# Kernel tuning notes

Measured on AMD Instinct MI355X. Metric: run time of the kernel, lower is better.

Reference implementation:

```python
import jax, jax.numpy as jnp
import numpy as np

N, L, H, E = 4, 4096, 8, 64
CHUNK = 128  # chunk size for the blocked causal scan
EPS = 1e-6


def elu_feature_map(x):
    # phi(x) = elu(x) + 1 (default feature map of fast-transformers)
    return jax.nn.elu(x) + 1.0


def causal_dot_product(Q, K, V, chunk=CHUNK):
    """out[n,l,h,:] = sum_{s<=l} (Q[n,l,h,:].K[n,s,h,:]) * V[n,s,h,:].
    Chunked scan over the [E,M] KV state: O(N L H E M) without an [L,L] matrix."""
    n, l, h, e = Q.shape
    m = V.shape[-1]
    nc = l // chunk

    def to_chunks(x):
        # [n, l, h, d] -> [nc, n, h, chunk, d]
        return x.reshape(n, nc, chunk, h, x.shape[-1]).transpose(1, 0, 3, 2, 4)

    q, k, v = to_chunks(Q), to_chunks(K), to_chunks(V)
    tril = jnp.tril(jnp.ones((chunk, chunk), dtype=Q.dtype))

    def step(S, xs):  # S: [n, h, e, m] running sum of k v^T
        qc, kc, vc = xs  # [n, h, chunk, e/m]
        inter = jnp.einsum('nhce,nhem->nhcm', qc, S)
        attn = jnp.einsum('nhce,nhde->nhcd', qc, kc) * tril  # intra-chunk causal
        intra = jnp.einsum('nhcd,nhdm->nhcm', attn, vc)
        S = S + jnp.einsum('nhce,nhcm->nhem', kc, vc)
        return S, inter + intra

    S0 = jnp.zeros((n, h, e, m), dtype=Q.dtype)
    _, out = jax.lax.scan(step, S0, (q, k, v))  # [nc, n, h, chunk, m]
    return out.transpose(1, 0, 3, 2, 4).reshape(n, l, h, m)


def setup_inputs() -> dict:
    key = jax.random.key(0)
    k1, k2, k3 = jax.random.split(key, 3)
    return {
        'queries': jax.random.normal(k1, (N, L, H, E), jnp.float32),
        'keys': jax.random.normal(k2, (N, L, H, E), jnp.float32),
        'values': jax.random.normal(k3, (N, L, H, E), jnp.float32),
        'key_lengths': jnp.ones((N, L), jnp.float32),  # float length mask
    }


def reference(queries, keys, values, key_lengths):
    Q = elu_feature_map(queries)
    K = elu_feature_map(keys) * key_lengths[:, :, None, None]
    # denominator: Z[n,l,h] = 1 / (Q[n,l,h] . cumsum_s<=l K[n,s,h] + eps)
    Z = 1.0 / (jnp.einsum('nlhe,nlhe->nlh', Q, jnp.cumsum(K, axis=1)) + EPS)
    V_new = causal_dot_product(Q, K, values)
    return V_new * Z[:, :, :, None]
```

## Files before the change

kernel.cpp:

```cpp
#include <hip/hip_runtime.h>
#include <math.h>

#define NN 4
#define LL 4096
#define HH 8
#define EE 64
#define CHK 128
#define SUB 64
#define NCH (LL/CHK)
#define NG (NN*HH*NCH)
#define EPSF 1e-6f

typedef float f32x4 __attribute__((ext_vector_type(4)));
typedef __bf16 bf16x8 __attribute__((ext_vector_type(8)));

__device__ __forceinline__ float phi_map(float x) {
  return x > 0.0f ? x + 1.0f : __expf(x);
}

#define MFMA(a, b, c) __builtin_amdgcn_mfma_f32_16x16x32_bf16((a), (b), (c), 0, 0, 0)

__device__ __forceinline__ int swz(int row, int d) {
  return row * 128 + (d & 7) + 8 * ((d >> 3) ^ ((row >> 2) & 7));
}
__device__ __forceinline__ int frag_off(int row, int ks, int lg) {
  return row * 128 + 8 * ((4 * ks + lg) ^ ((row >> 2) & 7));
}

__global__ __launch_bounds__(256) void k_chunksums(
    const float* __restrict__ Kg, const float* __restrict__ Vg,
    const float* __restrict__ KLg, __bf16* __restrict__ ScG, __bf16* __restrict__ KscG)
{
  __shared__ __bf16 sKt[64 * 128];
  __shared__ __bf16 sVt[64 * 128];
  const int g = blockIdx.x;
  const int c = g % NCH;
  const int nh = g / NCH;
  const int h = nh % HH;
  const int n = nh / HH;
  const int l0 = c * CHK;
  const int t = threadIdx.x;

  #pragma unroll
  for (int it = 0; it < 8; ++it) {
    int f = t + 256 * it;
    int d = f >> 4;
    int c4 = (f & 15) << 2;
    size_t gb = (((size_t)n * LL + (size_t)(l0 + d)) * HH + h) * EE + c4;
    float4 kk = *(const float4*)(Kg + gb);
    float4 vv = *(const float4*)(Vg + gb);
    float klr = KLg[n * LL + l0 + d];
    float ka[4] = {phi_map(kk.x) * klr, phi_map(kk.y) * klr,
                   phi_map(kk.z) * klr, phi_map(kk.w) * klr};
    float va[4] = {vv.x, vv.y, vv.z, vv.w};
    #pragma unroll
    for (int j = 0; j < 4; ++j) {
      sKt[swz(c4 + j, d)] = (__bf16)ka[j];
      sVt[swz(c4 + j, d)] = (__bf16)va[j];
    }
  }
  __syncthreads();

  const int w = t >> 6;
  const int lane = t & 63;
  const int lg = lane >> 4;
  const int li = lane & 15;

  bf16x8 aV[4];
  #pragma unroll
  for (int ks = 0; ks < 4; ++ks)
    aV[ks] = *(const bf16x8*)&sVt[frag_off(16 * w + li, ks, lg)];

  bf16x8 ones;
  #pragma unroll
  for (int i = 0; i < 8; ++i) ones[i] = (__bf16)1.0f;

  f32x4 acc[4], accK[4];
  #pragma unroll
  for (int nt = 0; nt < 4; ++nt) {
    acc[nt] = (f32x4){0.f, 0.f, 0.f, 0.f};
    accK[nt] = (f32x4){0.f, 0.f, 0.f, 0.f};
  }

  #pragma unroll
  for (int nt = 0; nt < 4; ++nt) {
    #pragma unroll
    for (int ks = 0; ks < 4; ++ks) {
      bf16x8 b = *(const bf16x8*)&sKt[frag_off(li + 16 * nt, ks, lg)];
      acc[nt] = MFMA(aV[ks], b, acc[nt]);
      if (w == 0) accK[nt] = MFMA(ones, b, accK[nt]);
    }
  }

  __bf16* sp = ScG + (size_t)g * 4096;
  #pragma unroll
  for (int nt = 0; nt < 4; ++nt)
    #pragma unroll
    for (int reg = 0; reg < 4; ++reg)
      sp[(16 * w + 4 * lg + reg) * 64 + li + 16 * nt] = (__bf16)acc[nt][reg];

  if (w == 0 && lg == 0) {
    #pragma unroll
    for (int nt = 0; nt < 4; ++nt)
      KscG[(size_t)g * 64 + li + 16 * nt] = (__bf16)accK[nt][0];
  }
}

__global__ __launch_bounds__(256) void k_prefix(
    const __bf16* __restrict__ Sc, __bf16* __restrict__ Sp,
    const __bf16* __restrict__ Ksc, __bf16* __restrict__ Ksp)
{
  const int bid = blockIdx.x;
  const int nh = bid >> 4;
  const int strip = bid & 15;
  const int t = threadIdx.x;
  const int entry = strip * 256 + t;
  float run = 0.0f;
  for (int c = 0; c < NCH; ++c) {
    size_t base = ((size_t)nh * NCH + c) * 4096 + entry;
    float v = (float)Sc[base];
    Sp[base] = (__bf16)run;
    run += v;
  }
  if (strip == 0 && t < 64) {
    float kr = 0.0f;
    for (int c = 0; c < NCH; ++c) {
      size_t kb = ((size_t)nh * NCH + c) * 64 + t;
      float v = (float)Ksc[kb];
      Ksp[kb] = (__bf16)kr;
      kr += v;
    }
  }
}

__global__ __launch_bounds__(256) void k_pass2(
    const float* __restrict__ Qg, const float* __restrict__ Kg,
    const float* __restrict__ Vg, const float* __restrict__ KLg,
    const __bf16* __restrict__ Sp, const __bf16* __restrict__ Ksp,
    float* __restrict__ Og)
{
  __shared__ __bf16 sK[2][64][72];
  __shared__ __bf16 sVt[2][64][72];
  __shared__ __bf16 sSt[80][72];
  __shared__ __bf16 sAt[4][16][72];

  const int g = blockIdx.x;
  const int c = g % NCH;
  const int nh = g / NCH;
  const int h = nh % HH;
  const int n = nh / HH;
  const int t = threadIdx.x;
  const int w = t >> 6;
  const int lane = t & 63;
  const int lg = lane >> 4;
  const int li = lane & 15;

  {
    const bf16x8* sp8 = (const bf16x8*)(Sp + (size_t)g * 4096);
    bf16x8 s0 = sp8[2 * t];
    bf16x8 s1 = sp8[2 * t + 1];
    int m = t >> 2;
    int e0 = (t & 3) * 16;
    *(bf16x8*)&sSt[m][e0] = s0;
    *(bf16x8*)&sSt[m][e0 + 8] = s1;
    if (t < 64) sSt[64][t] = Ksp[(size_t)g * 64 + t];
    for (int i = t; i < 15 * 72; i += 256) sSt[65 + i / 72][i % 72] = (__bf16)0.0f;
  }

  for (int s = 0; s < 2; ++s) {
    const int l0 = c * CHK + s * SUB;
    const int arow = 16 * w + li;

    const float* qrow = Qg + (((size_t)n * LL + (size_t)(l0 + arow)) * HH + h) * EE;
    float4 q0 = *(const float4*)(qrow + 8 * lg);
    float4 q1 = *(const float4*)(qrow + 8 * lg + 4);
    float4 q2 = *(const float4*)(qrow + 32 + 8 * lg);
    float4 q3 = *(const float4*)(qrow + 32 + 8 * lg + 4);

    #pragma unroll
    for (int it = 0; it < 4; ++it) {
      int f = t + 256 * it;
      int rr = f >> 4;
      int c4 = (f & 15) << 2;
      size_t gb = (((size_t)n * LL + (size_t)(l0 + rr)) * HH + h) * EE + c4;
      float4 kk = *(const float4*)(Kg + gb);
      float4 vv = *(const float4*)(Vg + gb);
      float klr = KLg[n * LL + l0 + rr];
      __bf16* kd = &sK[s][rr][c4];
      kd[0] = (__bf16)(phi_map(kk.x) * klr); kd[1] = (__bf16)(phi_map(kk.y) * klr);
      kd[2] = (__bf16)(phi_map(kk.z) * klr); kd[3] = (__bf16)(phi_map(kk.w) * klr);
      sVt[s][c4 + 0][rr] = (__bf16)vv.x;
      sVt[s][c4 + 1][rr] = (__bf16)vv.y;
      sVt[s][c4 + 2][rr] = (__bf16)vv.z;
      sVt[s][c4 + 3][rr] = (__bf16)vv.w;
    }

    bf16x8 aQ0, aQ1;
    aQ0[0] = (__bf16)phi_map(q0.x); aQ0[1] = (__bf16)phi_map(q0.y);
    aQ0[2] = (__bf16)phi_map(q0.z); aQ0[3] = (__bf16)phi_map(q0.w);
    aQ0[4] = (__bf16)phi_map(q1.x); aQ0[5] = (__bf16)phi_map(q1.y);
    aQ0[6] = (__bf16)phi_map(q1.z); aQ0[7] = (__bf16)phi_map(q1.w);
    aQ1[0] = (__bf16)phi_map(q2.x); aQ1[1] = (__bf16)phi_map(q2.y);
    aQ1[2] = (__bf16)phi_map(q2.z); aQ1[3] = (__bf16)phi_map(q2.w);
    aQ1[4] = (__bf16)phi_map(q3.x); aQ1[5] = (__bf16)phi_map(q3.y);
    aQ1[6] = (__bf16)phi_map(q3.z); aQ1[7] = (__bf16)phi_map(q3.w);

    __syncthreads();

    f32x4 acc[4];
    #pragma unroll
    for (int nt = 0; nt < 4; ++nt) acc[nt] = (f32x4){0.f, 0.f, 0.f, 0.f};
    f32x4 accden = (f32x4){0.f, 0.f, 0.f, 0.f};

    #pragma unroll
    for (int nt = 0; nt < 4; ++nt) {
      bf16x8 b0 = *(const bf16x8*)&sSt[li + 16 * nt][8 * lg];
      bf16x8 b1 = *(const bf16x8*)&sSt[li + 16 * nt][32 + 8 * lg];
      acc[nt] = MFMA(aQ0, b0, acc[nt]);
      acc[nt] = MFMA(aQ1, b1, acc[nt]);
    }
    {
      bf16x8 b0 = *(const bf16x8*)&sSt[64 + li][8 * lg];
      bf16x8 b1 = *(const bf16x8*)&sSt[64 + li][32 + 8 * lg];
      accden = MFMA(aQ0, b0, accden);
      accden = MFMA(aQ1, b1, accden);
    }
    float den[4];
    #pragma unroll
    for (int reg = 0; reg < 4; ++reg) den[reg] = __shfl(accden[reg], 16 * lg);

    float rs[4] = {0.f, 0.f, 0.f, 0.f};

    if (s == 1) {
      f32x4 cat[4];
      #pragma unroll
      for (int nt = 0; nt < 4; ++nt) cat[nt] = (f32x4){0.f, 0.f, 0.f, 0.f};
      #pragma unroll
      for (int nt = 0; nt < 4; ++nt) {
        bf16x8 b0 = *(const bf16x8*)&sK[0][li + 16 * nt][8 * lg];
        bf16x8 b1 = *(const bf16x8*)&sK[0][li + 16 * nt][32 + 8 * lg];
        cat[nt] = MFMA(aQ0, b0, cat[nt]);
        cat[nt] = MFMA(aQ1, b1, cat[nt]);
      }
      #pragma unroll
      for (int nt = 0; nt < 4; ++nt) {
        #pragma unroll
        for (int reg = 0; reg < 4; ++reg) {
          float av = cat[nt][reg];
          rs[reg] += av;
          sAt[w][4 * lg + reg][li + 16 * nt] = (__bf16)av;
        }
      }
      bf16x8 aC0 = *(const bf16x8*)&sAt[w][li][8 * lg];
      bf16x8 aC1 = *(const bf16x8*)&sAt[w][li][32 + 8 * lg];
      #pragma unroll
      for (int nt = 0; nt < 4; ++nt) {
        bf16x8 b0 = *(const bf16x8*)&sVt[0][li + 16 * nt][8 * lg];
        bf16x8 b1 = *(const bf16x8*)&sVt[0][li + 16 * nt][32 + 8 * lg];
        acc[nt] = MFMA(aC0, b0, acc[nt]);
        acc[nt] = MFMA(aC1, b1, acc[nt]);
      }
    }

    {
      f32x4 at2[4];
      #pragma unroll
      for (int nt = 0; nt < 4; ++nt) at2[nt] = (f32x4){0.f, 0.f, 0.f, 0.f};
      for (int nt = 0; nt <= w; ++nt) {
        bf16x8 b0 = *(const bf16x8*)&sK[s][li + 16 * nt][8 * lg];
        bf16x8 b1 = *(const bf16x8*)&sK[s][li + 16 * nt][32 + 8 * lg];
        at2[nt] = MFMA(aQ0, b0, at2[nt]);
        at2[nt] = MFMA(aQ1, b1, at2[nt]);
      }
      #pragma unroll
      for (int nt = 0; nt < 4; ++nt) {
        #pragma unroll
        for (int reg = 0; reg < 4; ++reg) {
          int row = 16 * w + 4 * lg + reg;
          int col = li + 16 * nt;
          float av = (nt <= w && col <= row) ? at2[nt][reg] : 0.0f;
          rs[reg] += av;
          sAt[w][4 * lg + reg][col] = (__bf16)av;
        }
      }
      bf16x8 aA0 = *(const bf16x8*)&sAt[w][li][8 * lg];
      bf16x8 aA1 = aA0;
      if (w >= 2) aA1 = *(const bf16x8*)&sAt[w][li][32 + 8 * lg];
      #pragma unroll
      for (int nt = 0; nt < 4; ++nt) {
        bf16x8 b0 = *(const bf16x8*)&sVt[s][li + 16 * nt][8 * lg];
        acc[nt] = MFMA(aA0, b0, acc[nt]);
        if (w >= 2) {
          bf16x8 b1 = *(const bf16x8*)&sVt[s][li + 16 * nt][32 + 8 * lg];
          acc[nt] = MFMA(aA1, b1, acc[nt]);
        }
      }
    }

    #pragma unroll
    for (int reg = 0; reg < 4; ++reg) {
      float v = rs[reg];
      v += __shfl_xor(v, 1);
      v += __shfl_xor(v, 2);
      v += __shfl_xor(v, 4);
      v += __shfl_xor(v, 8);
      rs[reg] = v;
    }

    #pragma unroll
    for (int reg = 0; reg < 4; ++reg) {
      float inv = 1.0f / (den[reg] + rs[reg] + EPSF);
      int row = l0 + 16 * w + 4 * lg + reg;
      size_t ob = (((size_t)n * LL + row) * HH + h) * EE + li;
      #pragma unroll
      for (int nt = 0; nt < 4; ++nt)
        Og[ob + 16 * nt] = acc[nt][reg] * inv;
    }
    __syncthreads();
  }
}

extern "C" void kernel_launch(void* const* d_in, const int* in_sizes, int n_in,
                              void* d_out, int out_size, void* d_ws, size_t ws_size,
                              hipStream_t stream) {
  const float* Qg  = (const float*)d_in[0];
  const float* Kg  = (const float*)d_in[1];
  const float* Vg  = (const float*)d_in[2];
  const float* KLg = (const float*)d_in[3];
  float* Og = (float*)d_out;

  __bf16* Sc  = (__bf16*)d_ws;
  __bf16* Sp  = (__bf16*)((char*)d_ws + (size_t)NG * 4096 * 2);
  __bf16* Ksc = (__bf16*)((char*)d_ws + (size_t)NG * 4096 * 4);
  __bf16* Ksp = (__bf16*)((char*)d_ws + (size_t)NG * 4096 * 4 + (size_t)NG * 64 * 2);

  hipLaunchKernelGGL(k_chunksums, dim3(NG), dim3(256), 0, stream, Kg, Vg, KLg, Sc, Ksc);
  hipLaunchKernelGGL(k_prefix, dim3(NN*HH*16), dim3(256), 0, stream, Sc, Sp, Ksc, Ksp);
  hipLaunchKernelGGL(k_pass2, dim3(NG), dim3(256), 0, stream, Qg, Kg, Vg, KLg, Sp, Ksp, Og);
}
```

Baseline: 53.09 us.

## Halve chunk size to 64, simplify pass2, and make the prefix scan in-place and batched

The scan chunk shrinks from 128 to 64, which doubles the block count in the chunk-sum and output kernels. Each pass2 block now handles a single 64-row sub-chunk, so the cross-sub-chunk branch and the double-buffered shared arrays go away and shared memory use drops enough for launch_bounds(256,6). The prefix kernel loads all chunk values into registers first and rewrites them in place, removing separate output buffers, and spreads the K-sum prefix across extra blocks. The denominator is now a per-lane dot product plus shuffles instead of an MFMA against a zero-padded tile. In exchange, the serial prefix has twice as many chunks, and twice as many chunk-state matrices are written and read through the workspace.

```diff
diff --git a/kernel.cpp b/kernel.cpp
--- a/kernel.cpp
+++ b/kernel.cpp
@@ -5,8 +5,7 @@
 #define LL 4096
 #define HH 8
 #define EE 64
-#define CHK 128
-#define SUB 64
+#define CHK 64
 #define NCH (LL/CHK)
 #define NG (NN*HH*NCH)
 #define EPSF 1e-6f
@@ -20,19 +19,19 @@
 
 #define MFMA(a, b, c) __builtin_amdgcn_mfma_f32_16x16x32_bf16((a), (b), (c), 0, 0, 0)
 
-__device__ __forceinline__ int swz(int row, int d) {
-  return row * 128 + (d & 7) + 8 * ((d >> 3) ^ ((row >> 2) & 7));
-}
-__device__ __forceinline__ int frag_off(int row, int ks, int lg) {
-  return row * 128 + 8 * ((4 * ks + lg) ^ ((row >> 2) & 7));
+__device__ __forceinline__ int swz64(int row, int d) {
+  return row * 64 + (d & 7) + 8 * ((d >> 3) ^ ((row >> 2) & 7));
+}
+__device__ __forceinline__ int frag64(int row, int blk) {
+  return row * 64 + 8 * (blk ^ ((row >> 2) & 7));
 }
 
 __global__ __launch_bounds__(256) void k_chunksums(
     const float* __restrict__ Kg, const float* __restrict__ Vg,
     const float* __restrict__ KLg, __bf16* __restrict__ ScG, __bf16* __restrict__ KscG)
 {
-  __shared__ __bf16 sKt[64 * 128];
-  __shared__ __bf16 sVt[64 * 128];
+  __shared__ __bf16 sKt[4096];
+  __shared__ __bf16 sVt[4096];
   const int g = blockIdx.x;
   const int c = g % NCH;
   const int nh = g / NCH;
@@ -42,7 +41,7 @@
   const int t = threadIdx.x;
 
   #pragma unroll
-  for (int it = 0; it < 8; ++it) {
+  for (int it = 0; it < 4; ++it) {
     int f = t + 256 * it;
     int d = f >> 4;
     int c4 = (f & 15) << 2;
@@ -55,8 +54,8 @@
     float va[4] = {vv.x, vv.y, vv.z, vv.w};
     #pragma unroll
     for (int j = 0; j < 4; ++j) {
-      sKt[swz(c4 + j, d)] = (__bf16)ka[j];
-      sVt[swz(c4 + j, d)] = (__bf16)va[j];
+      sKt[swz64(c4 + j, d)] = (__bf16)ka[j];
+      sVt[swz64(c4 + j, d)] = (__bf16)va[j];
     }
   }
   __syncthreads();
@@ -66,10 +65,10 @@
   const int lg = lane >> 4;
   const int li = lane & 15;
 
-  bf16x8 aV[4];
-  #pragma unroll
-  for (int ks = 0; ks < 4; ++ks)
-    aV[ks] = *(const bf16x8*)&sVt[frag_off(16 * w + li, ks, lg)];
+  bf16x8 aV[2];
+  #pragma unroll
+  for (int ks = 0; ks < 2; ++ks)
+    aV[ks] = *(const bf16x8*)&sVt[frag64(16 * w + li, 4 * ks + lg)];
 
   bf16x8 ones;
   #pragma unroll
@@ -85,8 +84,8 @@
   #pragma unroll
   for (int nt = 0; nt < 4; ++nt) {
     #pragma unroll
-    for (int ks = 0; ks < 4; ++ks) {
-      bf16x8 b = *(const bf16x8*)&sKt[frag_off(li + 16 * nt, ks, lg)];
+    for (int ks = 0; ks < 2; ++ks) {
+      bf16x8 b = *(const bf16x8*)&sKt[frag64(li + 16 * nt, 4 * ks + lg)];
       acc[nt] = MFMA(aV[ks], b, acc[nt]);
       if (w == 0) accK[nt] = MFMA(ones, b, accK[nt]);
     }
@@ -107,42 +106,50 @@
 }
 
 __global__ __launch_bounds__(256) void k_prefix(
-    const __bf16* __restrict__ Sc, __bf16* __restrict__ Sp,
-    const __bf16* __restrict__ Ksc, __bf16* __restrict__ Ksp)
+    __bf16* __restrict__ Sc, __bf16* __restrict__ Ksc)
 {
   const int bid = blockIdx.x;
-  const int nh = bid >> 4;
-  const int strip = bid & 15;
   const int t = threadIdx.x;
-  const int entry = strip * 256 + t;
-  float run = 0.0f;
-  for (int c = 0; c < NCH; ++c) {
-    size_t base = ((size_t)nh * NCH + c) * 4096 + entry;
-    float v = (float)Sc[base];
-    Sp[base] = (__bf16)run;
-    run += v;
-  }
-  if (strip == 0 && t < 64) {
-    float kr = 0.0f;
+  if (bid < NN * HH * 16) {
+    const int nh = bid >> 4;
+    const int strip = bid & 15;
+    const int entry = strip * 256 + t;
+    __bf16 v[NCH];
+    #pragma unroll
+    for (int c = 0; c < NCH; ++c)
+      v[c] = Sc[((size_t)(nh * NCH + c) << 12) + entry];
+    float run = 0.0f;
+    #pragma unroll
     for (int c = 0; c < NCH; ++c) {
-      size_t kb = ((size_t)nh * NCH + c) * 64 + t;
-      float v = (float)Ksc[kb];
-      Ksp[kb] = (__bf16)kr;
-      kr += v;
-    }
-  }
-}
-
-__global__ __launch_bounds__(256) void k_pass2(
+      Sc[((size_t)(nh * NCH + c) << 12) + entry] = (__bf16)run;
+      run += (float)v[c];
+    }
+  } else {
+    const int idx = (bid - NN * HH * 16) * 256 + t;
+    const int nh = idx >> 6;
+    const int e = idx & 63;
+    __bf16 v[NCH];
+    #pragma unroll
+    for (int c = 0; c < NCH; ++c)
+      v[c] = Ksc[((size_t)(nh * NCH + c) << 6) + e];
+    float run = 0.0f;
+    #pragma unroll
+    for (int c = 0; c < NCH; ++c) {
+      Ksc[((size_t)(nh * NCH + c) << 6) + e] = (__bf16)run;
+      run += (float)v[c];
+    }
+  }
+}
+
+__global__ __launch_bounds__(256, 6) void k_pass2(
     const float* __restrict__ Qg, const float* __restrict__ Kg,
     const float* __restrict__ Vg, const float* __restrict__ KLg,
     const __bf16* __restrict__ Sp, const __bf16* __restrict__ Ksp,
     float* __restrict__ Og)
 {
-  __shared__ __bf16 sK[2][64][72];
-  __shared__ __bf16 sVt[2][64][72];
-  __shared__ __bf16 sSt[80][72];
-  __shared__ __bf16 sAt[4][16][72];
+  __shared__ __bf16 sK[64][72];
+  __shared__ __bf16 sVt[4096];
+  __shared__ __bf16 sU[4608];
 
   const int g = blockIdx.x;
   const int c = g % NCH;
@@ -154,6 +161,7 @@
   const int lane = t & 63;
   const int lg = lane >> 4;
   const int li = lane & 15;
+  const int l0 = c * CHK;
 
   {
     const bf16x8* sp8 = (const bf16x8*)(Sp + (size_t)g * 4096);
@@ -161,162 +169,128 @@
     bf16x8 s1 = sp8[2 * t + 1];
     int m = t >> 2;
     int e0 = (t & 3) * 16;
-    *(bf16x8*)&sSt[m][e0] = s0;
-    *(bf16x8*)&sSt[m][e0 + 8] = s1;
-    if (t < 64) sSt[64][t] = Ksp[(size_t)g * 64 + t];
-    for (int i = t; i < 15 * 72; i += 256) sSt[65 + i / 72][i % 72] = (__bf16)0.0f;
-  }
-
-  for (int s = 0; s < 2; ++s) {
-    const int l0 = c * CHK + s * SUB;
-    const int arow = 16 * w + li;
-
-    const float* qrow = Qg + (((size_t)n * LL + (size_t)(l0 + arow)) * HH + h) * EE;
-    float4 q0 = *(const float4*)(qrow + 8 * lg);
-    float4 q1 = *(const float4*)(qrow + 8 * lg + 4);
-    float4 q2 = *(const float4*)(qrow + 32 + 8 * lg);
-    float4 q3 = *(const float4*)(qrow + 32 + 8 * lg + 4);
-
-    #pragma unroll
-    for (int it = 0; it < 4; ++it) {
-      int f = t + 256 * it;
-      int rr = f >> 4;
-      int c4 = (f & 15) << 2;
-      size_t gb = (((size_t)n * LL + (size_t)(l0 + rr)) * HH + h) * EE + c4;
-      float4 kk = *(const float4*)(Kg + gb);
-      float4 vv = *(const float4*)(Vg + gb);
-      float klr = KLg[n * LL + l0 + rr];
-      __bf16* kd = &sK[s][rr][c4];
-      kd[0] = (__bf16)(phi_map(kk.x) * klr); kd[1] = (__bf16)(phi_map(kk.y) * klr);
-      kd[2] = (__bf16)(phi_map(kk.z) * klr); kd[3] = (__bf16)(phi_map(kk.w) * klr);
-      sVt[s][c4 + 0][rr] = (__bf16)vv.x;
-      sVt[s][c4 + 1][rr] = (__bf16)vv.y;
-      sVt[s][c4 + 2][rr] = (__bf16)vv.z;
-      sVt[s][c4 + 3][rr] = (__bf16)vv.w;
-    }
-
-    bf16x8 aQ0, aQ1;
-    aQ0[0] = (__bf16)phi_map(q0.x); aQ0[1] = (__bf16)phi_map(q0.y);
-    aQ0[2] = (__bf16)phi_map(q0.z); aQ0[3] = (__bf16)phi_map(q0.w);
-    aQ0[4] = (__bf16)phi_map(q1.x); aQ0[5] = (__bf16)phi_map(q1.y);
-    aQ0[6] = (__bf16)phi_map(q1.z); aQ0[7] = (__bf16)phi_map(q1.w);
-    aQ1[0] = (__bf16)phi_map(q2.x); aQ1[1] = (__bf16)phi_map(q2.y);
-    aQ1[2] = (__bf16)phi_map(q2.z); aQ1[3] = (__bf16)phi_map(q2.w);
-    aQ1[4] = (__bf16)phi_map(q3.x); aQ1[5] = (__bf16)phi_map(q3.y);
-    aQ1[6] = (__bf16)phi_map(q3.z); aQ1[7] = (__bf16)phi_map(q3.w);
-
-    __syncthreads();
-
-    f32x4 acc[4];
-    #pragma unroll
-    for (int nt = 0; nt < 4; ++nt) acc[nt] = (f32x4){0.f, 0.f, 0.f, 0.f};
-    f32x4 accden = (f32x4){0.f, 0.f, 0.f, 0.f};
-
+    *(bf16x8*)&sU[m * 72 + e0] = s0;
+    *(bf16x8*)&sU[m * 72 + e0 + 8] = s1;
+  }
+
+  #pragma unroll
+  for (int it = 0; it < 4; ++it) {
+    int f = t + 256 * it;
+    int rr = f >> 4;
+    int c4 = (f & 15) << 2;
+    size_t gb = (((size_t)n * LL + (size_t)(l0 + rr)) * HH + h) * EE + c4;
+    float4 kk = *(const float4*)(Kg + gb);
+    float4 vv = *(const float4*)(Vg + gb);
+    float klr = KLg[n * LL + l0 + rr];
+    __bf16* kd = &sK[rr][c4];
+    kd[0] = (__bf16)(phi_map(kk.x) * klr); kd[1] = (__bf16)(phi_map(kk.y) * klr);
+    kd[2] = (__bf16)(phi_map(kk.z) * klr); kd[3] = (__bf16)(phi_map(kk.w) * klr);
+    float va[4] = {vv.x, vv.y, vv.z, vv.w};
+    #pragma unroll
+    for (int j = 0; j < 4; ++j)
+      sVt[swz64(c4 + j, rr)] = (__bf16)va[j];
+  }
+
+  const int arow = 16 * w + li;
+  const float* qrow = Qg + (((size_t)n * LL + (size_t)(l0 + arow)) * HH + h) * EE;
+  float4 q0 = *(const float4*)(qrow + 8 * lg);
+  float4 q1 = *(const float4*)(qrow + 8 * lg + 4);
+  float4 q2 = *(const float4*)(qrow + 32 + 8 * lg);
+  float4 q3 = *(const float4*)(qrow + 32 + 8 * lg + 4);
+  bf16x8 aQ0, aQ1;
+  aQ0[0] = (__bf16)phi_map(q0.x); aQ0[1] = (__bf16)phi_map(q0.y);
+  aQ0[2] = (__bf16)phi_map(q0.z); aQ0[3] = (__bf16)phi_map(q0.w);
+  aQ0[4] = (__bf16)phi_map(q1.x); aQ0[5] = (__bf16)phi_map(q1.y);
+  aQ0[6] = (__bf16)phi_map(q1.z); aQ0[7] = (__bf16)phi_map(q1.w);
+  aQ1[0] = (__bf16)phi_map(q2.x); aQ1[1] = (__bf16)phi_map(q2.y);
+  aQ1[2] = (__bf16)phi_map(q2.z); aQ1[3] = (__bf16)phi_map(q2.w);
+  aQ1[4] = (__bf16)phi_map(q3.x); aQ1[5] = (__bf16)phi_map(q3.y);
+  aQ1[6] = (__bf16)phi_map(q3.z); aQ1[7] = (__bf16)phi_map(q3.w);
+
+  const __bf16* kb = Ksp + (size_t)g * 64;
+  bf16x8 ks0 = *(const bf16x8*)(kb + 8 * lg);
+  bf16x8 ks1 = *(const bf16x8*)(kb + 32 + 8 * lg);
+
+  __syncthreads();
+
+  f32x4 acc[4];
+  #pragma unroll
+  for (int nt = 0; nt < 4; ++nt) acc[nt] = (f32x4){0.f, 0.f, 0.f, 0.f};
+  #pragma unroll
+  for (int nt = 0; nt < 4; ++nt) {
+    bf16x8 b0 = *(const bf16x8*)&sU[(li + 16 * nt) * 72 + 8 * lg];
+    bf16x8 b1 = *(const bf16x8*)&sU[(li + 16 * nt) * 72 + 32 + 8 * lg];
+    acc[nt] = MFMA(aQ0, b0, acc[nt]);
+    acc[nt] = MFMA(aQ1, b1, acc[nt]);
+  }
+
+  float dv = 0.0f;
+  #pragma unroll
+  for (int i = 0; i < 8; ++i) {
+    dv += (float)aQ0[i] * (float)ks0[i];
+    dv += (float)aQ1[i] * (float)ks1[i];
+  }
+  dv += __shfl_xor(dv, 16);
+  dv += __shfl_xor(dv, 32);
+  float den[4];
+  #pragma unroll
+  for (int reg = 0; reg < 4; ++reg) den[reg] = __shfl(dv, 4 * lg + reg);
+
+  __syncthreads();
+
+  float rs[4] = {0.f, 0.f, 0.f, 0.f};
+  #pragma unroll
+  for (int nt = 0; nt < 4; ++nt) {
+    f32x4 at2 = (f32x4){0.f, 0.f, 0.f, 0.f};
+    if (nt <= w) {
+      bf16x8 b0 = *(const bf16x8*)&sK[li + 16 * nt][8 * lg];
+      bf16x8 b1 = *(const bf16x8*)&sK[li + 16 * nt][32 + 8 * lg];
+      at2 = MFMA(aQ0, b0, at2);
+      at2 = MFMA(aQ1, b1, at2);
+    }
+    #pragma unroll
+    for (int reg = 0; reg < 4; ++reg) {
+      int row = 16 * w + 4 * lg + reg;
+      int col = li + 16 * nt;
+      float av = (col <= row) ? at2[reg] : 0.0f;
+      rs[reg] += av;
+      sU[w * 1152 + (4 * lg + reg) * 72 + col] = (__bf16)av;
+    }
+  }
+
+  {
+    bf16x8 aA0 = *(const bf16x8*)&sU[w * 1152 + li * 72 + 8 * lg];
+    bf16x8 aA1 = aA0;
+    if (w >= 2) aA1 = *(const bf16x8*)&sU[w * 1152 + li * 72 + 32 + 8 * lg];
     #pragma unroll
     for (int nt = 0; nt < 4; ++nt) {
-      bf16x8 b0 = *(const bf16x8*)&sSt[li + 16 * nt][8 * lg];
-      bf16x8 b1 = *(const bf16x8*)&sSt[li + 16 * nt][32 + 8 * lg];
-      acc[nt] = MFMA(aQ0, b0, acc[nt]);
-      acc[nt] = MFMA(aQ1, b1, acc[nt]);
-    }
-    {
-      bf16x8 b0 = *(const bf16x8*)&sSt[64 + li][8 * lg];
-      bf16x8 b1 = *(const bf16x8*)&sSt[64 + li][32 + 8 * lg];
-      accden = MFMA(aQ0, b0, accden);
-      accden = MFMA(aQ1, b1, accden);
-    }
-    float den[4];
-    #pragma unroll
-    for (int reg = 0; reg < 4; ++reg) den[reg] = __shfl(accden[reg], 16 * lg);
-
-    float rs[4] = {0.f, 0.f, 0.f, 0.f};
-
-    if (s == 1) {
-      f32x4 cat[4];
-      #pragma unroll
-      for (int nt = 0; nt < 4; ++nt) cat[nt] = (f32x4){0.f, 0.f, 0.f, 0.f};
-      #pragma unroll
-      for (int nt = 0; nt < 4; ++nt) {
-        bf16x8 b0 = *(const bf16x8*)&sK[0][li + 16 * nt][8 * lg];
-        bf16x8 b1 = *(const bf16x8*)&sK[0][li + 16 * nt][32 + 8 * lg];
-        cat[nt] = MFMA(aQ0, b0, cat[nt]);
-        cat[nt] = MFMA(aQ1, b1, cat[nt]);
+      bf16x8 bv0 = *(const bf16x8*)&sVt[frag64(li + 16 * nt, lg)];
+      acc[nt] = MFMA(aA0, bv0, acc[nt]);
+      if (w >= 2) {
+        bf16x8 bv1 = *(const bf16x8*)&sVt[frag64(li + 16 * nt, 4 + lg)];
+        acc[nt] = MFMA(aA1, bv1, acc[nt]);
       }
-      #pragma unroll
-      for (int nt = 0; nt < 4; ++nt) {
-        #pragma unroll
-        for (int reg = 0; reg < 4; ++reg) {
-          float av = cat[nt][reg];
-          rs[reg] += av;
-          sAt[w][4 * lg + reg][li + 16 * nt] = (__bf16)av;
-        }
-      }
-      bf16x8 aC0 = *(const bf16x8*)&sAt[w][li][8 * lg];
-      bf16x8 aC1 = *(const bf16x8*)&sAt[w][li][32 + 8 * lg];
-      #pragma unroll
-      for (int nt = 0; nt < 4; ++nt) {
-        bf16x8 b0 = *(const bf16x8*)&sVt[0][li + 16 * nt][8 * lg];
-        bf16x8 b1 = *(const bf16x8*)&sVt[0][li + 16 * nt][32 + 8 * lg];
-        acc[nt] = MFMA(aC0, b0, acc[nt]);
-        acc[nt] = MFMA(aC1, b1, acc[nt]);
-      }
-    }
-
-    {
-      f32x4 at2[4];
-      #pragma unroll
-      for (int nt = 0; nt < 4; ++nt) at2[nt] = (f32x4){0.f, 0.f, 0.f, 0.f};
-      for (int nt = 0; nt <= w; ++nt) {
-        bf16x8 b0 = *(const bf16x8*)&sK[s][li + 16 * nt][8 * lg];
-        bf16x8 b1 = *(const bf16x8*)&sK[s][li + 16 * nt][32 + 8 * lg];
-        at2[nt] = MFMA(aQ0, b0, at2[nt]);
-        at2[nt] = MFMA(aQ1, b1, at2[nt]);
-      }
-      #pragma unroll
-      for (int nt = 0; nt < 4; ++nt) {
-        #pragma unroll
-        for (int reg = 0; reg < 4; ++reg) {
-          int row = 16 * w + 4 * lg + reg;
-          int col = li + 16 * nt;
-          float av = (nt <= w && col <= row) ? at2[nt][reg] : 0.0f;
-          rs[reg] += av;
-          sAt[w][4 * lg + reg][col] = (__bf16)av;
-        }
-      }
-      bf16x8 aA0 = *(const bf16x8*)&sAt[w][li][8 * lg];
-      bf16x8 aA1 = aA0;
-      if (w >= 2) aA1 = *(const bf16x8*)&sAt[w][li][32 + 8 * lg];
-      #pragma unroll
-      for (int nt = 0; nt < 4; ++nt) {
-        bf16x8 b0 = *(const bf16x8*)&sVt[s][li + 16 * nt][8 * lg];
-        acc[nt] = MFMA(aA0, b0, acc[nt]);
-        if (w >= 2) {
-          bf16x8 b1 = *(const bf16x8*)&sVt[s][li + 16 * nt][32 + 8 * lg];
-          acc[nt] = MFMA(aA1, b1, acc[nt]);
-        }
-      }
-    }
-
-    #pragma unroll
-    for (int reg = 0; reg < 4; ++reg) {
-      float v = rs[reg];
-      v += __shfl_xor(v, 1);
-      v += __shfl_xor(v, 2);
-      v += __shfl_xor(v, 4);
-      v += __shfl_xor(v, 8);
-      rs[reg] = v;
-    }
-
-    #pragma unroll
-    for (int reg = 0; reg < 4; ++reg) {
-      float inv = 1.0f / (den[reg] + rs[reg] + EPSF);
-      int row = l0 + 16 * w + 4 * lg + reg;
-      size_t ob = (((size_t)n * LL + row) * HH + h) * EE + li;
-      #pragma unroll
-      for (int nt = 0; nt < 4; ++nt)
-        Og[ob + 16 * nt] = acc[nt][reg] * inv;
-    }
-    __syncthreads();
+    }
+  }
+
+  #pragma unroll
+  for (int reg = 0; reg < 4; ++reg) {
+    float v = rs[reg];
+    v += __shfl_xor(v, 1);
+    v += __shfl_xor(v, 2);
+    v += __shfl_xor(v, 4);
+    v += __shfl_xor(v, 8);
+    rs[reg] = v;
+  }
+
+  #pragma unroll
+  for (int reg = 0; reg < 4; ++reg) {
+    float inv = 1.0f / (den[reg] + rs[reg] + EPSF);
+    int row = l0 + 16 * w + 4 * lg + reg;
+    size_t ob = (((size_t)n * LL + row) * HH + h) * EE + li;
+    #pragma unroll
+    for (int nt = 0; nt < 4; ++nt)
+      Og[ob + 16 * nt] = acc[nt][reg] * inv;
   }
 }
 
@@ -330,11 +304,9 @@
   float* Og = (float*)d_out;
 
   __bf16* Sc  = (__bf16*)d_ws;
-  __bf16* Sp  = (__bf16*)((char*)d_ws + (size_t)NG * 4096 * 2);
-  __bf16* Ksc = (__bf16*)((char*)d_ws + (size_t)NG * 4096 * 4);
-  __bf16* Ksp = (__bf16*)((char*)d_ws + (size_t)NG * 4096 * 4 + (size_t)NG * 64 * 2);
+  __bf16* Ksc = (__bf16*)((char*)d_ws + (size_t)NG * 4096 * 2);
 
   hipLaunchKernelGGL(k_chunksums, dim3(NG), dim3(256), 0, stream, Kg, Vg, KLg, Sc, Ksc);
-  hipLaunchKernelGGL(k_prefix, dim3(NN*HH*16), dim3(256), 0, stream, Sc, Sp, Ksc, Ksp);
-  hipLaunchKernelGGL(k_pass2, dim3(NG), dim3(256), 0, stream, Qg, Kg, Vg, KLg, Sp, Ksp, Og);
-}
+  hipLaunchKernelGGL(k_prefix, dim3(NN*HH*16 + 8), dim3(256), 0, stream, Sc, Ksc);
+  hipLaunchKernelGGL(k_pass2, dim3(NG), dim3(256), 0, stream, Qg, Kg, Vg, KLg, Sc, Ksc, Og);
+}
```

Measured after the change: 51.34 us. 3.3% less time.
